# Performance work log

Measured on AMD Instinct MI355X. Metric: run time of the kernel, lower is better.

Reference implementation:

```python
import jax, jax.numpy as jnp
import numpy as np

S_DIM = 128            # attention head width s
E_DIM = 1024           # expansion e = 2*hidden
SQRT_S = 128.0 ** 0.5
EPS = 1e-5


def setup_inputs() -> dict:
    key = jax.random.key(0)
    ks = jax.random.split(key, 8)
    B, S, H = 64, 512, 512
    uv_dim = 2 * E_DIM + S_DIM  # 2176
    # xavier-uniform-ish scale for uv weight
    lim = (6.0 / (H + uv_dim)) ** 0.5
    return {
        "x": jax.random.normal(ks[0], (B, S, H), dtype=jnp.float32),
        "ln_g": jnp.ones((1,), dtype=jnp.float32),
        "uv_w": jax.random.uniform(ks[1], (uv_dim, H), minval=-lim, maxval=lim, dtype=jnp.float32),
        "uv_b": jnp.zeros((uv_dim,), dtype=jnp.float32),
        "gamma": jax.random.uniform(ks[2], (2, S_DIM), dtype=jnp.float32),
        "beta": jax.random.uniform(ks[3], (2, S_DIM), dtype=jnp.float32),
        "w_bias": jax.random.uniform(ks[4], (2 * S - 1,), dtype=jnp.float32),
        "o_w": jax.random.normal(ks[5], (H, E_DIM), dtype=jnp.float32) * 0.02,
        "o_b": jnp.zeros((H,), dtype=jnp.float32),
    }


def _rope(x):
    # x: [B, S, 2, s]; rotate along the sequence dim (dim=1)
    S = x.shape[1]
    half = x.shape[-1] // 2
    pos = jnp.arange(S, dtype=jnp.float32)
    # torch: freq_seq = -arange(half)/half; inv_freq = 10000**(-freq_seq)
    inv_freq = 10000.0 ** (jnp.arange(half, dtype=jnp.float32) / half)
    sinus = pos[:, None, None] * inv_freq[None, None, :]  # [S, 1, half]
    sin, cos = jnp.sin(sinus), jnp.cos(sinus)
    x1, x2 = x[..., :half], x[..., half:]
    return jnp.concatenate([x1 * cos - x2 * sin, x2 * cos + x1 * sin], axis=-1)


def reference(x, ln_g, uv_w, uv_b, gamma, beta, w_bias, o_w, o_b):
    B, S, H = x.shape
    # ScaleNorm
    norm = jnp.linalg.norm(x, axis=-1, keepdims=True) * (H ** -0.5)
    xn = x / jnp.maximum(norm, EPS) * ln_g
    # fused uv projection + SiLU
    act = jax.nn.silu(xn @ uv_w.T + uv_b)  # [B, S, 2e+s]
    u = act[..., :E_DIM]
    v = act[..., E_DIM:2 * E_DIM]
    base = act[..., 2 * E_DIM:]                      # [B, S, s]
    base = base[:, :, None, :] * gamma + beta        # [B, S, 2, s]
    base = _rope(base)
    q, k = base[:, :, 0, :], base[:, :, 1, :]
    # scores + relative position bias: bias[i, j] = w[j - i + S - 1]
    qk = jnp.einsum('bsd,btd->bst', q, k)
    idx = jnp.arange(S)[None, :] - jnp.arange(S)[:, None] + (S - 1)
    qk = qk + w_bias[idx]
    # relu2 similarity kernel
    kernel = jnp.square(jax.nn.relu(qk / SQRT_S))    # [B, S, S]
    out = u * jnp.einsum('bst,bte->bse', kernel, v)  # gated attention
    out = out @ o_w.T + o_b
    return out + x  # use_shortcut: hidden == output
```

## Files before the change

kernel.cpp:

```cpp
#include <hip/hip_runtime.h>
#include <math.h>


#define M_TOT   32768
#define S_LEN   512
#define H_DIM   512
#define E_DIMC  1024
#define UV_DIM  2176
#define D_DIM   128

using floatx4  = __attribute__((ext_vector_type(4))) float;
using uintx2   = __attribute__((ext_vector_type(2))) unsigned int;
using uintx4   = __attribute__((ext_vector_type(4))) unsigned int;
using ushortx4 = __attribute__((ext_vector_type(4))) unsigned short;
using short8   = __attribute__((ext_vector_type(8))) short;

#define ASYNC_CP16(gsrc, ldst)                                                  \
    __builtin_amdgcn_global_load_lds(                                           \
        (const __attribute__((address_space(1))) void*)(gsrc),                  \
        (__attribute__((address_space(3))) void*)(ldst), 16, 0, 0)

__device__ __forceinline__ float bf2f(unsigned short h) {
    union { unsigned int u; float f; } c;
    c.u = ((unsigned int)h) << 16;
    return c.f;
}
__device__ __forceinline__ unsigned short f2bf(float f) {
    union { float f; unsigned int u; } c;
    c.f = f;
    unsigned int r = c.u + 0x7fffu + ((c.u >> 16) & 1u);
    return (unsigned short)(r >> 16);
}
__device__ __forceinline__ float silu_fast(float x) {
    float e = __expf(-x);
    return x * __builtin_amdgcn_rcpf(1.0f + e);
}

__global__ __launch_bounds__(256) void f2bf_kernel(const float* __restrict__ in,
                                                   unsigned short* __restrict__ out,
                                                   int n4) {
    int i = blockIdx.x * 256 + threadIdx.x;
    if (i < n4) {
        floatx4 v = ((const floatx4*)in)[i];
        ushortx4 o;
        o.x = f2bf(v.x); o.y = f2bf(v.y); o.z = f2bf(v.z); o.w = f2bf(v.w);
        ((ushortx4*)out)[i] = o;
    }
}

__global__ __launch_bounds__(256) void rmsnorm_kernel(const float* __restrict__ x,
                                                      const float* __restrict__ ln_g,
                                                      unsigned short* __restrict__ xn) {
    int row  = blockIdx.x * 4 + (threadIdx.x >> 6);
    int lane = threadIdx.x & 63;
    const float* xr = x + (size_t)row * H_DIM;
    floatx4 v0 = ((const floatx4*)xr)[lane];
    floatx4 v1 = ((const floatx4*)xr)[lane + 64];
    float ss = v0.x*v0.x + v0.y*v0.y + v0.z*v0.z + v0.w*v0.w
             + v1.x*v1.x + v1.y*v1.y + v1.z*v1.z + v1.w*v1.w;
    #pragma unroll
    for (int off = 32; off > 0; off >>= 1) ss += __shfl_xor(ss, off, 64);
    float norm = sqrtf(ss) * 0.044194173824159216f;
    float sc   = ln_g[0] / fmaxf(norm, 1e-5f);
    unsigned short* xo = xn + (size_t)row * H_DIM;
    ushortx4 o0, o1;
    o0.x = f2bf(v0.x * sc); o0.y = f2bf(v0.y * sc);
    o0.z = f2bf(v0.z * sc); o0.w = f2bf(v0.w * sc);
    o1.x = f2bf(v1.x * sc); o1.y = f2bf(v1.y * sc);
    o1.z = f2bf(v1.z * sc); o1.w = f2bf(v1.w * sc);
    ((ushortx4*)xo)[lane]      = o0;
    ((ushortx4*)xo)[lane + 64] = o1;
}

__global__ __launch_bounds__(64) void rope_table_kernel(float* __restrict__ cost,
                                                        float* __restrict__ sint) {
    int s = blockIdx.x;
    int j = threadIdx.x;
    float invf = (float)pow(10000.0, (double)j / 64.0);
    float ang  = (float)s * invf;
    double a   = (double)ang;
    cost[s * 64 + j] = (float)cos(a);
    sint[s * 64 + j] = (float)sin(a);
}

__global__ __launch_bounds__(256) void rope_apply_kernel(const float* __restrict__ base,
                                                         const float* __restrict__ gamma,
                                                         const float* __restrict__ beta,
                                                         const float* __restrict__ cost,
                                                         const float* __restrict__ sint,
                                                         unsigned short* __restrict__ q,
                                                         unsigned short* __restrict__ k) {
    int idx = blockIdx.x * 256 + threadIdx.x;
    int m = idx >> 6;
    int j = idx & 63;
    int s = m & (S_LEN - 1);
    float b1 = base[(size_t)m * D_DIM + j];
    float b2 = base[(size_t)m * D_DIM + 64 + j];
    float c  = cost[s * 64 + j];
    float sn = sint[s * 64 + j];
    float yq1 = b1 * gamma[j]       + beta[j];
    float yq2 = b2 * gamma[64 + j]  + beta[64 + j];
    float yk1 = b1 * gamma[128 + j] + beta[128 + j];
    float yk2 = b2 * gamma[192 + j] + beta[192 + j];
    q[(size_t)m * D_DIM + j]      = f2bf(yq1 * c - yq2 * sn);
    q[(size_t)m * D_DIM + 64 + j] = f2bf(yq2 * c + yq1 * sn);
    k[(size_t)m * D_DIM + j]      = f2bf(yk1 * c - yk2 * sn);
    k[(size_t)m * D_DIM + 64 + j] = f2bf(yk2 * c + yk1 * sn);
}

struct GemmLds {
    unsigned short As[128 * 64];
    unsigned short Bs[128 * 64];
};

__device__ __forceinline__ void gemm_bt_core(const unsigned short* __restrict__ A,
                                             const unsigned short* __restrict__ B,
                                             int lda, int ldb, int K,
                                             int m0, int n0,
                                             GemmLds& lds, floatx4 (&acc)[4][4]) {
    const int tid  = threadIdx.x;
    const int lane = tid & 63;
    const int wave = tid >> 6;
    const int quad = lane >> 4;
    const int l16  = lane & 15;
    const int wm   = (wave >> 1) * 64;
    const int wn   = (wave & 1) * 64;
    const int lrow = lane >> 3;
    const int cgs  = ((lane & 7) ^ lrow) * 8;

    #pragma unroll
    for (int i = 0; i < 4; i++)
        #pragma unroll
        for (int j = 0; j < 4; j++) acc[i][j] = (floatx4){0.f, 0.f, 0.f, 0.f};

    for (int kt = 0; kt < K; kt += 64) {
        #pragma unroll
        for (int i = 0; i < 4; i++) {
            int r0 = wave * 32 + i * 8;
            const unsigned short* ga = A + (size_t)(m0 + r0 + lrow) * lda + kt + cgs;
            const unsigned short* gb = B + (size_t)(n0 + r0 + lrow) * ldb + kt + cgs;
            ASYNC_CP16(ga, &lds.As[r0 * 64]);
            ASYNC_CP16(gb, &lds.Bs[r0 * 64]);
        }
        __syncthreads();
        #pragma unroll
        for (int kk = 0; kk < 64; kk += 32) {
            short8 af[4], bf[4];
            const int pc = (kk + quad * 8) ^ ((l16 & 7) * 8);
            #pragma unroll
            for (int mt = 0; mt < 4; mt++) {
                int row = wm + mt * 16 + l16;
                union { short8 s8; uintx4 u4; } fu;
                fu.u4 = *(const uintx4*)&lds.As[row * 64 + pc];
                af[mt] = fu.s8;
            }
            #pragma unroll
            for (int nt = 0; nt < 4; nt++) {
                int row = wn + nt * 16 + l16;
                union { short8 s8; uintx4 u4; } fu;
                fu.u4 = *(const uintx4*)&lds.Bs[row * 64 + pc];
                bf[nt] = fu.s8;
            }
            #pragma unroll
            for (int mt = 0; mt < 4; mt++)
                #pragma unroll
                for (int nt = 0; nt < 4; nt++)
                    acc[mt][nt] = __builtin_amdgcn_mfma_f32_16x16x32_bf16(
                        af[mt], bf[nt], acc[mt][nt], 0, 0, 0);
        }
        __syncthreads();
    }
}

__global__ __launch_bounds__(256) void gemm1_kernel(const unsigned short* __restrict__ xn,
                                                    const unsigned short* __restrict__ uvw,
                                                    const float* __restrict__ uvb,
                                                    unsigned short* __restrict__ u,
                                                    unsigned short* __restrict__ vT,
                                                    float* __restrict__ base) {
    __shared__ union LdsU {
        GemmLds g;
        unsigned short T[128 * 136];
    } lds;
    floatx4 acc[4][4];
    const int m0 = blockIdx.x * 128, n0 = blockIdx.y * 128;
    gemm_bt_core(xn, uvw, H_DIM, H_DIM, H_DIM, m0, n0, lds.g, acc);

    const int tid  = threadIdx.x;
    const int lane = tid & 63;
    const int wave = tid >> 6;
    const int quad = lane >> 4;
    const int l16  = lane & 15;
    const int wm   = (wave >> 1) * 64;
    const int wn   = (wave & 1) * 64;

    if (blockIdx.y < 8) {
        #pragma unroll
        for (int mt = 0; mt < 4; mt++)
            #pragma unroll
            for (int nt = 0; nt < 4; nt++)
                #pragma unroll
                for (int r = 0; r < 4; r++) {
                    int m = m0 + wm + mt * 16 + quad * 4 + r;
                    int n = n0 + wn + nt * 16 + l16;
                    float val = acc[mt][nt][r] + uvb[n];
                    u[(size_t)m * E_DIMC + n] = f2bf(silu_fast(val));
                }
    } else if (blockIdx.y == 16) {
        #pragma unroll
        for (int mt = 0; mt < 4; mt++)
            #pragma unroll
            for (int nt = 0; nt < 4; nt++)
                #pragma unroll
                for (int r = 0; r < 4; r++) {
                    int m = m0 + wm + mt * 16 + quad * 4 + r;
                    int n = n0 + wn + nt * 16 + l16;
                    float val = acc[mt][nt][r] + uvb[n];
                    base[(size_t)m * D_DIM + (n - 2 * E_DIMC)] = silu_fast(val);
                }
    } else {
        #pragma unroll
        for (int mt = 0; mt < 4; mt++)
            #pragma unroll
            for (int nt = 0; nt < 4; nt++)
                #pragma unroll
                for (int r = 0; r < 4; r++) {
                    int ml = wm + mt * 16 + quad * 4 + r;
                    int nl = wn + nt * 16 + l16;
                    float val = acc[mt][nt][r] + uvb[n0 + nl];
                    lds.T[nl * 136 + ml] = f2bf(silu_fast(val));
                }
        __syncthreads();
        const int b   = m0 >> 9;
        const int sg0 = m0 & (S_LEN - 1);
        const int eg0 = n0 - E_DIMC;
        #pragma unroll
        for (int i = 0; i < 8; i++) {
            int idx = tid + i * 256;
            int e   = idx >> 4;
            int s8  = (idx & 15) * 8;
            uintx4 val = *(const uintx4*)&lds.T[e * 136 + s8];
            *(uintx4*)(vT + ((size_t)b * E_DIMC + eg0 + e) * S_LEN + sg0 + s8) = val;
        }
    }
}

__global__ __launch_bounds__(256) void gemm_qk_kernel(const unsigned short* __restrict__ q,
                                                      const unsigned short* __restrict__ k,
                                                      const float* __restrict__ wbias,
                                                      unsigned short* __restrict__ P) {
    __shared__ GemmLds lds;
    floatx4 acc[4][4];
    size_t boff = (size_t)blockIdx.z * S_LEN * D_DIM;
    unsigned short* Pb = P + (size_t)blockIdx.z * S_LEN * S_LEN;
    const int m0 = blockIdx.x * 128, n0 = blockIdx.y * 128;
    gemm_bt_core(q + boff, k + boff, D_DIM, D_DIM, D_DIM, m0, n0, lds, acc);

    const int tid = threadIdx.x, lane = tid & 63, wave = tid >> 6;
    const int quad = lane >> 4, l16 = lane & 15;
    const int wm = (wave >> 1) * 64, wn = (wave & 1) * 64;
    #pragma unroll
    for (int mt = 0; mt < 4; mt++)
        #pragma unroll
        for (int nt = 0; nt < 4; nt++)
            #pragma unroll
            for (int r = 0; r < 4; r++) {
                int s = m0 + wm + mt * 16 + quad * 4 + r;
                int t = n0 + wn + nt * 16 + l16;
                float z = (acc[mt][nt][r] + wbias[t - s + (S_LEN - 1)]) * 0.08838834764831845f;
                z = fmaxf(z, 0.f);
                Pb[(size_t)s * S_LEN + t] = f2bf(z * z);
            }
}

__global__ __launch_bounds__(256) void gemm_pv_kernel(const unsigned short* __restrict__ P,
                                                      const unsigned short* __restrict__ vT,
                                                      unsigned short* __restrict__ u) {
    __shared__ GemmLds lds;
    floatx4 acc[4][4];
    int bb = blockIdx.z;
    const unsigned short* Pb  = P  + (size_t)bb * S_LEN * S_LEN;
    const unsigned short* vTb = vT + (size_t)bb * E_DIMC * S_LEN;
    const int m0 = blockIdx.x * 128, n0 = blockIdx.y * 128;
    gemm_bt_core(Pb, vTb, S_LEN, S_LEN, S_LEN, m0, n0, lds, acc);

    const int tid = threadIdx.x, lane = tid & 63, wave = tid >> 6;
    const int quad = lane >> 4, l16 = lane & 15;
    const int wm = (wave >> 1) * 64, wn = (wave & 1) * 64;
    #pragma unroll
    for (int mt = 0; mt < 4; mt++)
        #pragma unroll
        for (int nt = 0; nt < 4; nt++)
            #pragma unroll
            for (int r = 0; r < 4; r++) {
                int s = m0 + wm + mt * 16 + quad * 4 + r;
                int e = n0 + wn + nt * 16 + l16;
                size_t off = ((size_t)bb * S_LEN + s) * E_DIMC + e;
                u[off] = f2bf(acc[mt][nt][r] * bf2f(u[off]));
            }
}

__global__ __launch_bounds__(256) void gemm_out_kernel(const unsigned short* __restrict__ oe,
                                                       const unsigned short* __restrict__ ow,
                                                       const float* __restrict__ ob,
                                                       const float* __restrict__ x,
                                                       float* __restrict__ out) {
    __shared__ GemmLds lds;
    floatx4 acc[4][4];
    const int m0 = blockIdx.x * 128, n0 = blockIdx.y * 128;
    gemm_bt_core(oe, ow, E_DIMC, E_DIMC, E_DIMC, m0, n0, lds, acc);

    const int tid = threadIdx.x, lane = tid & 63, wave = tid >> 6;
    const int quad = lane >> 4, l16 = lane & 15;
    const int wm = (wave >> 1) * 64, wn = (wave & 1) * 64;
    #pragma unroll
    for (int mt = 0; mt < 4; mt++)
        #pragma unroll
        for (int nt = 0; nt < 4; nt++)
            #pragma unroll
            for (int r = 0; r < 4; r++) {
                int m = m0 + wm + mt * 16 + quad * 4 + r;
                int n = n0 + wn + nt * 16 + l16;
                size_t off = (size_t)m * H_DIM + n;
                out[off] = acc[mt][nt][r] + ob[n] + x[off];
            }
}

extern "C" void kernel_launch(void* const* d_in, const int* in_sizes, int n_in,
                              void* d_out, int out_size, void* d_ws, size_t ws_size,
                              hipStream_t stream) {
    const float* x     = (const float*)d_in[0];
    const float* ln_g  = (const float*)d_in[1];
    const float* uv_w  = (const float*)d_in[2];
    const float* uv_b  = (const float*)d_in[3];
    const float* gamma = (const float*)d_in[4];
    const float* beta  = (const float*)d_in[5];
    const float* wbias = (const float*)d_in[6];
    const float* o_w   = (const float*)d_in[7];
    const float* o_b   = (const float*)d_in[8];
    float* out = (float*)d_out;

    char* ws = (char*)d_ws;
    size_t off = 0;
    auto alloc = [&](size_t bytes) {
        void* p = ws + off;
        off += (bytes + 255) & ~(size_t)255;
        return p;
    };
    unsigned short* u     = (unsigned short*)alloc((size_t)M_TOT * E_DIMC * 2);
    unsigned short* vT    = (unsigned short*)alloc((size_t)64 * E_DIMC * S_LEN * 2);
    unsigned short* xn    = (unsigned short*)alloc((size_t)M_TOT * H_DIM * 2);
    unsigned short* P     = xn;
    float*          base  = (float*)alloc((size_t)M_TOT * D_DIM * 4);
    unsigned short* q     = (unsigned short*)alloc((size_t)M_TOT * D_DIM * 2);
    unsigned short* k     = (unsigned short*)alloc((size_t)M_TOT * D_DIM * 2);
    float*          cost  = (float*)alloc((size_t)S_LEN * 64 * 4);
    float*          sint  = (float*)alloc((size_t)S_LEN * 64 * 4);
    unsigned short* uvwb  = (unsigned short*)alloc((size_t)UV_DIM * H_DIM * 2);
    unsigned short* owb   = (unsigned short*)alloc((size_t)H_DIM * E_DIMC * 2);
    (void)ws_size; (void)in_sizes; (void)n_in; (void)out_size;

    f2bf_kernel<<<(UV_DIM * H_DIM / 4 + 255) / 256, 256, 0, stream>>>(uv_w, uvwb, UV_DIM * H_DIM / 4);
    f2bf_kernel<<<(H_DIM * E_DIMC / 4 + 255) / 256, 256, 0, stream>>>(o_w, owb, H_DIM * E_DIMC / 4);
    rope_table_kernel<<<S_LEN, 64, 0, stream>>>(cost, sint);

    rmsnorm_kernel<<<M_TOT / 4, 256, 0, stream>>>(x, ln_g, xn);

    gemm1_kernel<<<dim3(M_TOT / 128, UV_DIM / 128), 256, 0, stream>>>(xn, uvwb, uv_b, u, vT, base);

    rope_apply_kernel<<<M_TOT * 64 / 256, 256, 0, stream>>>(base, gamma, beta, cost, sint, q, k);

    gemm_qk_kernel<<<dim3(S_LEN / 128, S_LEN / 128, 64), 256, 0, stream>>>(q, k, wbias, P);

    gemm_pv_kernel<<<dim3(S_LEN / 128, E_DIMC / 128, 64), 256, 0, stream>>>(P, vT, u);

    gemm_out_kernel<<<dim3(M_TOT / 128, H_DIM / 128), 256, 0, stream>>>(u, owb, o_b, x, out);
}
```

Measured before the change: 401.2 us.

## Coalesce GEMM epilogue stores via MFMA operand swap and LDS staging

Adds a template flag that swaps the MFMA A/B operands, so each lane holds four consecutive output columns instead of four rows. The epilogues of the u, QK, PV and output GEMMs then pack these values and stage them through LDS, and write them back as 16-byte row-contiguous stores instead of scattered 2- or 4-byte stores. gemm1 is split into a u kernel and a v/base kernel so each can use the layout that suits its output. The cost is extra LDS traffic, extra barriers and one more kernel launch.

```diff
diff --git a/kernel.cpp b/kernel.cpp
--- a/kernel.cpp
+++ b/kernel.cpp
@@ -113,6 +113,7 @@
     unsigned short Bs[128 * 64];
 };
 
+template <bool SWAPT>
 __device__ __forceinline__ void gemm_bt_core(const unsigned short* __restrict__ A,
                                              const unsigned short* __restrict__ B,
                                              int lda, int ldb, int K,
@@ -165,48 +166,97 @@
             for (int mt = 0; mt < 4; mt++)
                 #pragma unroll
                 for (int nt = 0; nt < 4; nt++)
-                    acc[mt][nt] = __builtin_amdgcn_mfma_f32_16x16x32_bf16(
-                        af[mt], bf[nt], acc[mt][nt], 0, 0, 0);
+                    acc[mt][nt] = SWAPT
+                        ? __builtin_amdgcn_mfma_f32_16x16x32_bf16(bf[nt], af[mt], acc[mt][nt], 0, 0, 0)
+                        : __builtin_amdgcn_mfma_f32_16x16x32_bf16(af[mt], bf[nt], acc[mt][nt], 0, 0, 0);
         }
         __syncthreads();
     }
 }
 
-__global__ __launch_bounds__(256) void gemm1_kernel(const unsigned short* __restrict__ xn,
-                                                    const unsigned short* __restrict__ uvw,
-                                                    const float* __restrict__ uvb,
-                                                    unsigned short* __restrict__ u,
-                                                    unsigned short* __restrict__ vT,
-                                                    float* __restrict__ base) {
-    __shared__ union LdsU {
-        GemmLds g;
-        unsigned short T[128 * 136];
-    } lds;
+union LdsU {
+    GemmLds g;
+    unsigned short T[128 * 136];
+};
+
+__global__ __launch_bounds__(256) void gemm1_u_kernel(const unsigned short* __restrict__ xn,
+                                                      const unsigned short* __restrict__ uvw,
+                                                      const float* __restrict__ uvb,
+                                                      unsigned short* __restrict__ u) {
+    __shared__ LdsU lds;
     floatx4 acc[4][4];
     const int m0 = blockIdx.x * 128, n0 = blockIdx.y * 128;
-    gemm_bt_core(xn, uvw, H_DIM, H_DIM, H_DIM, m0, n0, lds.g, acc);
-
-    const int tid  = threadIdx.x;
-    const int lane = tid & 63;
-    const int wave = tid >> 6;
-    const int quad = lane >> 4;
-    const int l16  = lane & 15;
-    const int wm   = (wave >> 1) * 64;
-    const int wn   = (wave & 1) * 64;
+    gemm_bt_core<true>(xn, uvw, H_DIM, H_DIM, H_DIM, m0, n0, lds.g, acc);
+
+    const int tid = threadIdx.x, lane = tid & 63, wave = tid >> 6;
+    const int quad = lane >> 4, l16 = lane & 15;
+    const int wm = (wave >> 1) * 64, wn = (wave & 1) * 64;
+
+    #pragma unroll
+    for (int mt = 0; mt < 4; mt++)
+        #pragma unroll
+        for (int nt = 0; nt < 4; nt++) {
+            int nl = wn + nt * 16 + quad * 4;
+            floatx4 b4 = *(const floatx4*)&uvb[n0 + nl];
+            ushortx4 pk;
+            #pragma unroll
+            for (int r = 0; r < 4; r++)
+                pk[r] = f2bf(silu_fast(acc[mt][nt][r] + b4[r]));
+            *(uintx2*)&lds.T[(wm + mt * 16 + l16) * 136 + nl] = *(uintx2*)&pk;
+        }
+    __syncthreads();
+    #pragma unroll
+    for (int i = 0; i < 8; i++) {
+        int idx = tid + i * 256;
+        int row = idx >> 4;
+        int c8  = (idx & 15) * 8;
+        *(uintx4*)(u + (size_t)(m0 + row) * E_DIMC + n0 + c8) =
+            *(const uintx4*)&lds.T[row * 136 + c8];
+    }
+}
+
+__global__ __launch_bounds__(256) void gemm1_vbase_kernel(const unsigned short* __restrict__ xn,
+                                                          const unsigned short* __restrict__ uvw,
+                                                          const float* __restrict__ uvb,
+                                                          unsigned short* __restrict__ vT,
+                                                          float* __restrict__ base) {
+    __shared__ LdsU lds;
+    floatx4 acc[4][4];
+    const int m0 = blockIdx.x * 128;
+    const int n0 = E_DIMC + blockIdx.y * 128;
+    gemm_bt_core<false>(xn, uvw, H_DIM, H_DIM, H_DIM, m0, n0, lds.g, acc);
+
+    const int tid = threadIdx.x, lane = tid & 63, wave = tid >> 6;
+    const int quad = lane >> 4, l16 = lane & 15;
+    const int wm = (wave >> 1) * 64, wn = (wave & 1) * 64;
 
     if (blockIdx.y < 8) {
         #pragma unroll
-        for (int mt = 0; mt < 4; mt++)
-            #pragma unroll
-            for (int nt = 0; nt < 4; nt++)
+        for (int nt = 0; nt < 4; nt++) {
+            int nl = wn + nt * 16 + l16;
+            float bias = uvb[n0 + nl];
+            #pragma unroll
+            for (int mt = 0; mt < 4; mt++) {
+                ushortx4 pk;
                 #pragma unroll
-                for (int r = 0; r < 4; r++) {
-                    int m = m0 + wm + mt * 16 + quad * 4 + r;
-                    int n = n0 + wn + nt * 16 + l16;
-                    float val = acc[mt][nt][r] + uvb[n];
-                    u[(size_t)m * E_DIMC + n] = f2bf(silu_fast(val));
-                }
-    } else if (blockIdx.y == 16) {
+                for (int r = 0; r < 4; r++)
+                    pk[r] = f2bf(silu_fast(acc[mt][nt][r] + bias));
+                *(uintx2*)&lds.T[nl * 136 + wm + mt * 16 + quad * 4] = *(uintx2*)&pk;
+            }
+        }
+        __syncthreads();
+        const int b   = m0 >> 9;
+        const int sg0 = m0 & (S_LEN - 1);
+        const int eg0 = n0 - E_DIMC;
+        #pragma unroll
+        for (int i = 0; i < 8; i++) {
+            int idx = tid + i * 256;
+            int e   = idx >> 4;
+            int s8  = (idx & 15) * 8;
+            *(uintx4*)(vT + ((size_t)b * E_DIMC + eg0 + e) * S_LEN + sg0 + s8) =
+                *(const uintx4*)&lds.T[e * 136 + s8];
+        }
+    } else {
         #pragma unroll
         for (int mt = 0; mt < 4; mt++)
             #pragma unroll
@@ -218,30 +268,6 @@
                     float val = acc[mt][nt][r] + uvb[n];
                     base[(size_t)m * D_DIM + (n - 2 * E_DIMC)] = silu_fast(val);
                 }
-    } else {
-        #pragma unroll
-        for (int mt = 0; mt < 4; mt++)
-            #pragma unroll
-            for (int nt = 0; nt < 4; nt++)
-                #pragma unroll
-                for (int r = 0; r < 4; r++) {
-                    int ml = wm + mt * 16 + quad * 4 + r;
-                    int nl = wn + nt * 16 + l16;
-                    float val = acc[mt][nt][r] + uvb[n0 + nl];
-                    lds.T[nl * 136 + ml] = f2bf(silu_fast(val));
-                }
-        __syncthreads();
-        const int b   = m0 >> 9;
-        const int sg0 = m0 & (S_LEN - 1);
-        const int eg0 = n0 - E_DIMC;
-        #pragma unroll
-        for (int i = 0; i < 8; i++) {
-            int idx = tid + i * 256;
-            int e   = idx >> 4;
-            int s8  = (idx & 15) * 8;
-            uintx4 val = *(const uintx4*)&lds.T[e * 136 + s8];
-            *(uintx4*)(vT + ((size_t)b * E_DIMC + eg0 + e) * S_LEN + sg0 + s8) = val;
-        }
     }
 }
 
@@ -249,40 +275,54 @@
                                                       const unsigned short* __restrict__ k,
                                                       const float* __restrict__ wbias,
                                                       unsigned short* __restrict__ P) {
-    __shared__ GemmLds lds;
+    __shared__ LdsU lds;
     floatx4 acc[4][4];
     size_t boff = (size_t)blockIdx.z * S_LEN * D_DIM;
     unsigned short* Pb = P + (size_t)blockIdx.z * S_LEN * S_LEN;
     const int m0 = blockIdx.x * 128, n0 = blockIdx.y * 128;
-    gemm_bt_core(q + boff, k + boff, D_DIM, D_DIM, D_DIM, m0, n0, lds, acc);
+    gemm_bt_core<true>(q + boff, k + boff, D_DIM, D_DIM, D_DIM, m0, n0, lds.g, acc);
 
     const int tid = threadIdx.x, lane = tid & 63, wave = tid >> 6;
     const int quad = lane >> 4, l16 = lane & 15;
     const int wm = (wave >> 1) * 64, wn = (wave & 1) * 64;
     #pragma unroll
-    for (int mt = 0; mt < 4; mt++)
-        #pragma unroll
-        for (int nt = 0; nt < 4; nt++)
+    for (int mt = 0; mt < 4; mt++) {
+        int s = m0 + wm + mt * 16 + l16;
+        #pragma unroll
+        for (int nt = 0; nt < 4; nt++) {
+            int nl = wn + nt * 16 + quad * 4;
+            int t0 = n0 + nl;
+            ushortx4 pk;
             #pragma unroll
             for (int r = 0; r < 4; r++) {
-                int s = m0 + wm + mt * 16 + quad * 4 + r;
-                int t = n0 + wn + nt * 16 + l16;
-                float z = (acc[mt][nt][r] + wbias[t - s + (S_LEN - 1)]) * 0.08838834764831845f;
+                float z = (acc[mt][nt][r] + wbias[t0 + r - s + (S_LEN - 1)]) * 0.08838834764831845f;
                 z = fmaxf(z, 0.f);
-                Pb[(size_t)s * S_LEN + t] = f2bf(z * z);
+                pk[r] = f2bf(z * z);
             }
+            *(uintx2*)&lds.T[(wm + mt * 16 + l16) * 136 + nl] = *(uintx2*)&pk;
+        }
+    }
+    __syncthreads();
+    #pragma unroll
+    for (int i = 0; i < 8; i++) {
+        int idx = tid + i * 256;
+        int row = idx >> 4;
+        int c8  = (idx & 15) * 8;
+        *(uintx4*)(Pb + (size_t)(m0 + row) * S_LEN + n0 + c8) =
+            *(const uintx4*)&lds.T[row * 136 + c8];
+    }
 }
 
 __global__ __launch_bounds__(256) void gemm_pv_kernel(const unsigned short* __restrict__ P,
                                                       const unsigned short* __restrict__ vT,
                                                       unsigned short* __restrict__ u) {
-    __shared__ GemmLds lds;
+    __shared__ LdsU lds;
     floatx4 acc[4][4];
     int bb = blockIdx.z;
     const unsigned short* Pb  = P  + (size_t)bb * S_LEN * S_LEN;
     const unsigned short* vTb = vT + (size_t)bb * E_DIMC * S_LEN;
     const int m0 = blockIdx.x * 128, n0 = blockIdx.y * 128;
-    gemm_bt_core(Pb, vTb, S_LEN, S_LEN, S_LEN, m0, n0, lds, acc);
+    gemm_bt_core<true>(Pb, vTb, S_LEN, S_LEN, S_LEN, m0, n0, lds.g, acc);
 
     const int tid = threadIdx.x, lane = tid & 63, wave = tid >> 6;
     const int quad = lane >> 4, l16 = lane & 15;
@@ -290,14 +330,27 @@
     #pragma unroll
     for (int mt = 0; mt < 4; mt++)
         #pragma unroll
-        for (int nt = 0; nt < 4; nt++)
-            #pragma unroll
-            for (int r = 0; r < 4; r++) {
-                int s = m0 + wm + mt * 16 + quad * 4 + r;
-                int e = n0 + wn + nt * 16 + l16;
-                size_t off = ((size_t)bb * S_LEN + s) * E_DIMC + e;
-                u[off] = f2bf(acc[mt][nt][r] * bf2f(u[off]));
-            }
+        for (int nt = 0; nt < 4; nt++) {
+            int nl = wn + nt * 16 + quad * 4;
+            ushortx4 pk;
+            #pragma unroll
+            for (int r = 0; r < 4; r++) pk[r] = f2bf(acc[mt][nt][r]);
+            *(uintx2*)&lds.T[(wm + mt * 16 + l16) * 136 + nl] = *(uintx2*)&pk;
+        }
+    __syncthreads();
+    #pragma unroll
+    for (int i = 0; i < 8; i++) {
+        int idx = tid + i * 256;
+        int row = idx >> 4;
+        int c8  = (idx & 15) * 8;
+        size_t off = ((size_t)bb * S_LEN + m0 + row) * E_DIMC + n0 + c8;
+        union { uintx4 u4; unsigned short s[8]; } tv, uv, ov;
+        tv.u4 = *(const uintx4*)&lds.T[row * 136 + c8];
+        uv.u4 = *(const uintx4*)(u + off);
+        #pragma unroll
+        for (int j = 0; j < 8; j++) ov.s[j] = f2bf(bf2f(tv.s[j]) * bf2f(uv.s[j]));
+        *(uintx4*)(u + off) = ov.u4;
+    }
 }
 
 __global__ __launch_bounds__(256) void gemm_out_kernel(const unsigned short* __restrict__ oe,
@@ -305,25 +358,43 @@
                                                        const float* __restrict__ ob,
                                                        const float* __restrict__ x,
                                                        float* __restrict__ out) {
-    __shared__ GemmLds lds;
+    __shared__ union {
+        GemmLds g;
+        float Tf[128 * 68];
+    } lds;
     floatx4 acc[4][4];
     const int m0 = blockIdx.x * 128, n0 = blockIdx.y * 128;
-    gemm_bt_core(oe, ow, E_DIMC, E_DIMC, E_DIMC, m0, n0, lds, acc);
+    gemm_bt_core<true>(oe, ow, E_DIMC, E_DIMC, E_DIMC, m0, n0, lds.g, acc);
 
     const int tid = threadIdx.x, lane = tid & 63, wave = tid >> 6;
     const int quad = lane >> 4, l16 = lane & 15;
-    const int wm = (wave >> 1) * 64, wn = (wave & 1) * 64;
-    #pragma unroll
-    for (int mt = 0; mt < 4; mt++)
-        #pragma unroll
-        for (int nt = 0; nt < 4; nt++)
-            #pragma unroll
-            for (int r = 0; r < 4; r++) {
-                int m = m0 + wm + mt * 16 + quad * 4 + r;
-                int n = n0 + wn + nt * 16 + l16;
-                size_t off = (size_t)m * H_DIM + n;
-                out[off] = acc[mt][nt][r] + ob[n] + x[off];
-            }
+    const int wm = (wave >> 1) * 64;
+
+    #pragma unroll
+    for (int h = 0; h < 2; h++) {
+        if ((wave & 1) == h) {
+            #pragma unroll
+            for (int mt = 0; mt < 4; mt++)
+                #pragma unroll
+                for (int nt = 0; nt < 4; nt++)
+                    *(floatx4*)&lds.Tf[(wm + mt * 16 + l16) * 68 + nt * 16 + quad * 4] =
+                        acc[mt][nt];
+        }
+        __syncthreads();
+        #pragma unroll
+        for (int i = 0; i < 8; i++) {
+            int idx = tid + i * 256;
+            int row = idx >> 4;
+            int c4  = (idx & 15) * 4;
+            int n   = n0 + h * 64 + c4;
+            floatx4 val = *(const floatx4*)&lds.Tf[row * 68 + c4];
+            floatx4 b4  = *(const floatx4*)&ob[n];
+            floatx4 x4  = *(const floatx4*)&x[(size_t)(m0 + row) * H_DIM + n];
+            val = val + b4 + x4;
+            *(floatx4*)&out[(size_t)(m0 + row) * H_DIM + n] = val;
+        }
+        __syncthreads();
+    }
 }
 
 extern "C" void kernel_launch(void* const* d_in, const int* in_sizes, int n_in,
@@ -366,7 +437,8 @@
 
     rmsnorm_kernel<<<M_TOT / 4, 256, 0, stream>>>(x, ln_g, xn);
 
-    gemm1_kernel<<<dim3(M_TOT / 128, UV_DIM / 128), 256, 0, stream>>>(xn, uvwb, uv_b, u, vT, base);
+    gemm1_u_kernel<<<dim3(M_TOT / 128, 8), 256, 0, stream>>>(xn, uvwb, uv_b, u);
+    gemm1_vbase_kernel<<<dim3(M_TOT / 128, 9), 256, 0, stream>>>(xn, uvwb, uv_b, vT, base);
 
     rope_apply_kernel<<<M_TOT * 64 / 256, 256, 0, stream>>>(base, gamma, beta, cost, sint, q, k);
 
```

After: 427.9 us. 1.07x slower.
